# Performance work log

Measured on AMD Instinct MI355X. Metric: run time of the kernel, lower is better.

Reference implementation:

```python
import jax, jax.numpy as jnp
import numpy as np

K = 16
EPS = 1e-5
NEG_SLOPE = 0.2


def leaky(x):
    return jnp.where(x > 0, x, NEG_SLOPE * x)


def batchnorm_train(x, gamma, beta):
    # x: [B, D]; training-mode BN with biased variance (torch semantics)
    mean = jnp.mean(x, axis=0)
    var = jnp.mean((x - mean) ** 2, axis=0)
    return (x - mean) * jax.lax.rsqrt(var + EPS) * gamma + beta


def setup_inputs() -> dict:
    key = jax.random.key(0)
    ks = jax.random.split(key, 20)
    N, M, D = 30000, 8000, 16
    s = lambda fan_in: 1.0 / np.sqrt(fan_in)
    inp = {
        "xyz": jax.random.normal(ks[0], (N, 3), jnp.float32),
        "atom_xyz": jax.random.normal(ks[1], (M, 3), jnp.float32),
        "atom_types": jax.random.normal(ks[2], (M, D), jnp.float32),
        "Wt1": jax.random.uniform(ks[3], (D, D), jnp.float32, -s(D), s(D)),
        "bt1": jax.random.uniform(ks[4], (D,), jnp.float32, -s(D), s(D)),
        "Wt2": jax.random.uniform(ks[5], (D, D), jnp.float32, -s(D), s(D)),
        "bt2": jax.random.uniform(ks[6], (D,), jnp.float32, -s(D), s(D)),
        "Wt3": jax.random.uniform(ks[7], (D, D), jnp.float32, -s(D), s(D)),
        "bt3": jax.random.uniform(ks[8], (D,), jnp.float32, -s(D), s(D)),
        # embed: conv1 Linear(D+1, D), conv2 Linear(D, D), conv3 Linear(2D, D)
        "W1": jax.random.uniform(ks[9], (D + 1, D), jnp.float32, -s(D + 1), s(D + 1)),
        "b1": jax.random.uniform(ks[10], (D,), jnp.float32, -s(D + 1), s(D + 1)),
        "W2": jax.random.uniform(ks[11], (D, D), jnp.float32, -s(D), s(D)),
        "b2": jax.random.uniform(ks[12], (D,), jnp.float32, -s(D), s(D)),
        "W3": jax.random.uniform(ks[13], (2 * D, D), jnp.float32, -s(2 * D), s(2 * D)),
        "b3": jax.random.uniform(ks[14], (D,), jnp.float32, -s(2 * D), s(2 * D)),
        # batchnorm affine params
        "g1": jnp.ones((D,), jnp.float32),
        "be1": jnp.zeros((D,), jnp.float32),
        "g2": jnp.ones((D,), jnp.float32),
        "be2": jnp.zeros((D,), jnp.float32),
    }
    return inp


def reference(xyz, atom_xyz, atom_types,
              Wt1, bt1, Wt2, bt2, Wt3, bt3,
              W1, b1, W2, b2, W3, b3, g1, be1, g2, be2):
    N, D = xyz.shape[0], atom_types.shape[1]

    # transform_types MLP on atom features: [M, D]
    t = leaky(atom_types @ Wt1 + bt1)
    t = leaky(t @ Wt2 + bt2)
    t = leaky(t @ Wt3 + bt3)

    # kNN: squared distances via GEMM expansion (avoids [N,M,3])
    d2 = (jnp.sum(xyz ** 2, axis=1, keepdims=True)
          + jnp.sum(atom_xyz ** 2, axis=1)[None, :]
          - 2.0 * xyz @ atom_xyz.T)                      # [N, M]
    _, idx = jax.lax.top_k(-d2, K)                       # [N, K] nearest atoms

    # gather neighbor coords, recompute exact squared dists (as in source)
    y_ik = atom_xyz[idx]                                 # [N, K, 3]
    dists = jnp.sum((xyz[:, None, :] - y_ik) ** 2, axis=-1)  # [N, K]

    feat = jnp.concatenate([t[idx], (1.0 / dists)[..., None]], axis=-1)  # [N,K,D+1]

    # conv1 -> leaky -> bn1 -> sum-pool
    fx = feat @ W1 + b1                                  # [N, K, D]
    fx = batchnorm_train(leaky(fx).reshape(-1, D), g1, be1).reshape(N, K, D)
    fx1 = fx.sum(axis=1)                                 # [N, D]

    # conv2 -> leaky -> bn2 -> sum-pool
    fx = fx @ W2 + b2
    fx = batchnorm_train(leaky(fx).reshape(-1, D), g2, be2).reshape(N, K, D)
    fx2 = fx.sum(axis=1)                                 # [N, D]

    return jnp.concatenate([fx1, fx2], axis=-1) @ W3 + b3  # [N, D]
```

## Files before the change

### kernel.cpp

```cpp
#include <hip/hip_runtime.h>

#define N_PTS   30000
#define M_ATOMS 8000
#define D       16
#define KNN     16
#define NGRP    125
#define EPS     1e-5f
#define SLOPE   0.2f
#define BN_COUNT 480000.0f

typedef unsigned long long ull;

__device__ __forceinline__ float leaky(float x) { return x > 0.f ? x : SLOPE * x; }

__device__ __forceinline__ unsigned fkey(float f) {
  unsigned u = __float_as_uint(f);
  return u ^ ((u & 0x80000000u) ? 0xFFFFFFFFu : 0x80000000u);
}
__device__ __forceinline__ float unfkey(unsigned e) {
  unsigned u = (e & 0x80000000u) ? (e ^ 0x80000000u) : ~e;
  return __uint_as_float(u);
}

#define DPPSTEP32(v, CTRL) {                                                   \
  unsigned t_ = (unsigned)__builtin_amdgcn_update_dpp(-1, (int)(v), CTRL, 0xF, 0xF, false); \
  (v) = t_ < (v) ? t_ : (v); }

__device__ __forceinline__ unsigned wmin32d(unsigned v) {
  DPPSTEP32(v, 0x111); DPPSTEP32(v, 0x112); DPPSTEP32(v, 0x114);
  DPPSTEP32(v, 0x118); DPPSTEP32(v, 0x142); DPPSTEP32(v, 0x143);
  return (unsigned)__builtin_amdgcn_readlane((int)v, 63);
}

__device__ __forceinline__ void cswap(ull& a, ull& b) {
  ull mn = a < b ? a : b, mx = a < b ? b : a;
  a = mn; b = mx;
}

__device__ __forceinline__ int morton_cell(float x, float y, float z) {
  int cx = min(max((int)floorf((x + 4.f) * 2.f), 0), 15);
  int cy = min(max((int)floorf((y + 4.f) * 2.f), 0), 15);
  int cz = min(max((int)floorf((z + 4.f) * 2.f), 0), 15);
  int c = 0;
#pragma unroll
  for (int b = 0; b < 4; ++b)
    c |= (((cx>>b)&1) << (3*b)) | (((cy>>b)&1) << (3*b+1)) | (((cz>>b)&1) << (3*b+2));
  return c;
}

#define LAYER(IN, OUT, W, B)                                        \
  _Pragma("unroll") for (int j = 0; j < 16; ++j) {                  \
    float acc = B[j];                                               \
    _Pragma("unroll") for (int i = 0; i < 16; ++i)                  \
      acc = fmaf(IN[i], W[i*16+j], acc);                            \
    OUT[j] = leaky(acc);                                            \
  }

__global__ void __launch_bounds__(256) kA_mlp_hist(
    const float* __restrict__ atom_xyz, const float* __restrict__ atom_types,
    const float* __restrict__ Wt1, const float* __restrict__ bt1,
    const float* __restrict__ Wt2, const float* __restrict__ bt2,
    const float* __restrict__ Wt3, const float* __restrict__ bt3,
    const float* __restrict__ W1, const float* __restrict__ b1,
    float* __restrict__ tu_out, int* __restrict__ hist) {
  __shared__ float w1[256], w2[256], w3[256], wc[256];
  __shared__ float bb1[16], bb2[16], bb3[16], bbc[16];
  __shared__ int lh[4096];
  int tid = threadIdx.x;
  for (int i = tid; i < 4096; i += 256) lh[i] = 0;
  w1[tid] = Wt1[tid]; w2[tid] = Wt2[tid]; w3[tid] = Wt3[tid]; wc[tid] = W1[tid];
  if (tid < 16) { bb1[tid] = bt1[tid]; bb2[tid] = bt2[tid];
                  bb3[tid] = bt3[tid]; bbc[tid] = b1[tid]; }
  __syncthreads();
  int m = blockIdx.x * 256 + tid;
  if (m < M_ATOMS) {
    int c = morton_cell(atom_xyz[m*3], atom_xyz[m*3+1], atom_xyz[m*3+2]);
    atomicAdd(&lh[c], 1);

    float u[16], v[16];
    const float4* tp = (const float4*)(atom_types + (size_t)m*16);
    float4 q0 = tp[0], q1 = tp[1], q2 = tp[2], q3 = tp[3];
    u[0]=q0.x; u[1]=q0.y; u[2]=q0.z; u[3]=q0.w;
    u[4]=q1.x; u[5]=q1.y; u[6]=q1.z; u[7]=q1.w;
    u[8]=q2.x; u[9]=q2.y; u[10]=q2.z; u[11]=q2.w;
    u[12]=q3.x; u[13]=q3.y; u[14]=q3.z; u[15]=q3.w;
    LAYER(u, v, w1, bb1);
    LAYER(v, u, w2, bb2);
    LAYER(u, v, w3, bb3);
    float up[16];
#pragma unroll
    for (int j = 0; j < 16; ++j) {
      float acc = bbc[j];
#pragma unroll
      for (int i = 0; i < 16; ++i) acc = fmaf(v[i], wc[i*16+j], acc);
      up[j] = acc;
    }
    float4* op = (float4*)(tu_out + (size_t)m*16);
    op[0] = make_float4(up[0], up[1], up[2], up[3]);
    op[1] = make_float4(up[4], up[5], up[6], up[7]);
    op[2] = make_float4(up[8], up[9], up[10], up[11]);
    op[3] = make_float4(up[12], up[13], up[14], up[15]);
  }
  __syncthreads();
  int* slice = hist + (size_t)blockIdx.x * 4096;
  for (int i = tid; i < 4096; i += 256) slice[i] = lh[i];
}

__global__ void __launch_bounds__(1024) kB_scan(
    const int* __restrict__ hist, int* __restrict__ cursors,
    float* __restrict__ gstats, unsigned* __restrict__ benc) {
  __shared__ int h0[4096], h1[4096];
  int tid = threadIdx.x;
  for (int i = tid; i < 4096; i += 1024) {
    int s = 0;
#pragma unroll
    for (int b = 0; b < 32; ++b) s += hist[b*4096 + i];
    h0[i] = s;
  }
  if (tid < 544) gstats[tid] = 0.f;
  if (tid < 375) benc[tid] = 0xFFFFFFFFu;
  if (tid >= 375 && tid < 750) benc[tid] = 0u;
  __syncthreads();
  int* src = h0; int* dst = h1;
  for (int off = 1; off < 4096; off <<= 1) {
    for (int i = tid; i < 4096; i += 1024) {
      int v = src[i];
      if (i >= off) v += src[i-off];
      dst[i] = v;
    }
    __syncthreads();
    int* t = src; src = dst; dst = t;
  }
  for (int i = tid; i < 4096; i += 1024) cursors[i] = i ? src[i-1] : 0;
}

__global__ void __launch_bounds__(256) kC_scatter(
    const float* __restrict__ atom_xyz, int* __restrict__ cursors,
    float4* __restrict__ atoms4s, int* __restrict__ origid,
    unsigned* __restrict__ benc) {
  int m = blockIdx.x * 256 + threadIdx.x;
  if (m >= M_ATOMS) return;
  float x = atom_xyz[m*3], y = atom_xyz[m*3+1], z = atom_xyz[m*3+2];
  int c = morton_cell(x, y, z);
  int pos = atomicAdd(&cursors[c], 1);
  atoms4s[pos] = make_float4(x, y, z, fmaf(x,x, fmaf(y,y, z*z)));
  origid[pos] = m;
  int g = pos >> 6;
  atomicMin(&benc[g],       fkey(x)); atomicMax(&benc[375+g],     fkey(x));
  atomicMin(&benc[125+g],   fkey(y)); atomicMax(&benc[375+125+g], fkey(y));
  atomicMin(&benc[250+g],   fkey(z)); atomicMax(&benc[375+250+g], fkey(z));
}

__global__ void __launch_bounds__(128) k_dec(
    const unsigned* __restrict__ benc, float4* __restrict__ bounds) {
  int g = threadIdx.x;
  if (g >= NGRP) return;
  bounds[2*g]   = make_float4(unfkey(benc[g]),     unfkey(benc[125+g]),
                              unfkey(benc[250+g]), 0.f);
  bounds[2*g+1] = make_float4(unfkey(benc[375+g]),     unfkey(benc[375+125+g]),
                              unfkey(benc[375+250+g]), 0.f);
}

__global__ void __launch_bounds__(128) k2_knn(
    const float* __restrict__ xyz, const float4* __restrict__ atoms4s,
    const int* __restrict__ origid, const float4* __restrict__ bounds,
    const float* __restrict__ atom_xyz, const float* __restrict__ tu,
    const float* __restrict__ W1,
    int2* __restrict__ pairs, float* __restrict__ gstats) {
  __shared__ float sbuf[2*16*20];
  int tid = threadIdx.x;
  int lane = tid & 63;
  int wid = tid >> 6;
  int n = blockIdx.x * 2 + wid;

  float px = xyz[n*3+0], py = xyz[n*3+1], pz = xyz[n*3+2];
  float x2 = fmaf(px,px, fmaf(py,py, pz*pz));

  unsigned ea, eb = 0xFFFFFFFFu;
  {
    int g = lane;
    float4 mn = bounds[2*g], mx = bounds[2*g+1];
    float dx = fmaxf(fmaxf(mn.x - px, px - mx.x), 0.f);
    float dy = fmaxf(fmaxf(mn.y - py, py - mx.y), 0.f);
    float dz = fmaxf(fmaxf(mn.z - pz, pz - mx.z), 0.f);
    float lb = fmaf(dx,dx, fmaf(dy,dy, dz*dz)) * 0.999f - 1e-4f;
    ea = (fkey(lb) & 0xFFFFFF00u) | (unsigned)g;
  }
  if (lane + 64 < NGRP) {
    int g = lane + 64;
    float4 mn = bounds[2*g], mx = bounds[2*g+1];
    float dx = fmaxf(fmaxf(mn.x - px, px - mx.x), 0.f);
    float dy = fmaxf(fmaxf(mn.y - py, py - mx.y), 0.f);
    float dz = fmaxf(fmaxf(mn.z - pz, pz - mx.z), 0.f);
    float lb = fmaf(dx,dx, fmaf(dy,dy, dz*dz)) * 0.999f - 1e-4f;
    eb = (fkey(lb) & 0xFFFFFF00u) | (unsigned)g;
  }
  unsigned cur = ea < eb ? ea : eb;
  unsigned bak = ea < eb ? eb : ea;

  int gs[4];
#pragma unroll
  for (int r = 0; r < 4; ++r) {
    unsigned m = wmin32d(cur);
    bool own = (cur == m);
    cur = own ? bak : cur;
    bak = own ? 0xFFFFFFFFu : bak;
    gs[r] = (int)(m & 0xFFu);
  }

  float4 A[4]; int OI[4];
#pragma unroll
  for (int r = 0; r < 4; ++r) {
    int base = gs[r] << 6;
    A[r]  = atoms4s[base + lane];
    OI[r] = origid [base + lane];
  }
  ull E[4];
#pragma unroll
  for (int r = 0; r < 4; ++r) {
    float dotp = fmaf(px,A[r].x, fmaf(py,A[r].y, pz*A[r].z));
    float d2 = (x2 + A[r].w) - 2.f*dotp;
    E[r] = ((ull)fkey(d2) << 32) | (unsigned)OI[r];
  }
  cswap(E[0],E[1]); cswap(E[2],E[3]); cswap(E[0],E[2]);
  cswap(E[1],E[3]); cswap(E[1],E[2]);
  unsigned cf0 = (unsigned)(E[0] >> 32), ci0 = (unsigned)E[0];
  unsigned cf1 = (unsigned)(E[1] >> 32), ci1 = (unsigned)E[1];
  unsigned cf2 = (unsigned)(E[2] >> 32), ci2 = (unsigned)E[2];
  unsigned cf3 = (unsigned)(E[3] >> 32), ci3 = (unsigned)E[3];

  ull res = ~0ull;
  unsigned mf = 0, mi = 0;
  for (int r = 0; r < KNN; ++r) {
    mf = wmin32d(cf0);
    ull ball = __ballot(cf0 == mf);
    if (__popcll(ball) == 1) {
      int srcl = (int)(__ffsll(ball) - 1);
      mi = (unsigned)__builtin_amdgcn_readlane((int)ci0, srcl);
    } else {
      unsigned cand = (cf0 == mf) ? ci0 : 0xFFFFFFFFu;
      mi = wmin32d(cand);
    }
    bool own = (cf0 == mf) && (ci0 == mi);
    if (lane == r) res = (((ull)mf) << 32) | mi;
    cf0 = own ? cf1 : cf0; cf1 = own ? cf2 : cf1;
    cf2 = own ? cf3 : cf2; cf3 = own ? 0xFFFFFFFFu : cf3;
    ci0 = own ? ci1 : ci0; ci1 = own ? ci2 : ci1;
    ci2 = own ? ci3 : ci2; ci3 = own ? 0xFFFFFFFFu : ci3;
  }
  ull lv = res;
  ull thresh = (((ull)mf) << 32) | mi;

  for (int it = 0; it < NGRP - 4; ++it) {
    unsigned m = wmin32d(cur);
    if ((m & 0xFFFFFF00u) >= (unsigned)(thresh >> 32)) break;
    bool own = (cur == m);
    cur = own ? bak : cur;
    bak = own ? 0xFFFFFFFFu : bak;
    int base = (int)(m & 0xFFu) << 6;

    float4 a = atoms4s[base + lane];
    int oi2 = origid[base + lane];
    float dotp = fmaf(px,a.x, fmaf(py,a.y, pz*a.z));
    float d2 = (x2 + a.w) - 2.f*dotp;
    ull key = ((ull)fkey(d2) << 32) | (unsigned)oi2;

    ull mk = __ballot(key < thresh);
    while (mk) {
      int src = (int)(__ffsll(mk) - 1);
      mk &= mk - 1;
      unsigned klo = (unsigned)__builtin_amdgcn_readlane((int)(unsigned)key, src);
      unsigned khi = (unsigned)__builtin_amdgcn_readlane((int)(unsigned)(key >> 32), src);
      ull kc = ((ull)khi << 32) | klo;
      if (kc < thresh) {
        bool ins = (lane < KNN) && (kc < lv);
        unsigned pvlo = (unsigned)__builtin_amdgcn_update_dpp(0, (int)(unsigned)lv,        0x111, 0xF, 0xF, false);
        unsigned pvhi = (unsigned)__builtin_amdgcn_update_dpp(0, (int)(unsigned)(lv>>32), 0x111, 0xF, 0xF, false);
        int pins      =           __builtin_amdgcn_update_dpp(0, ins ? 1 : 0,              0x111, 0xF, 0xF, false);
        if (ins) lv = pins ? (((ull)pvhi << 32) | pvlo) : kc;
        unsigned tlo = (unsigned)__builtin_amdgcn_readlane((int)(unsigned)lv, KNN-1);
        unsigned thi = (unsigned)__builtin_amdgcn_readlane((int)(unsigned)(lv >> 32), KNN-1);
        thresh = ((ull)thi << 32) | tlo;
      }
    }
  }

  int oi = (int)(unsigned)(lv & 0xFFFFFFFFull);
  float iv = 0.f;
  if (lane < KNN) {
    float bx = atom_xyz[oi*3+0], by = atom_xyz[oi*3+1], bz = atom_xyz[oi*3+2];
    float dx = px - bx, dy = py - by, dz = pz - bz;
    float dd = fmaf(dx,dx, fmaf(dy,dy, dz*dz));
    iv = 1.f / dd;
    pairs[n*KNN + lane] = make_int2(oi, __float_as_int(iv));

    const float4* up4 = (const float4*)(tu + (size_t)oi*16);
    float4 u0 = up4[0], u1 = up4[1], u2 = up4[2], u3 = up4[3];
    float4* row = (float4*)&sbuf[(wid*16 + lane)*20];
    float4 w;
    w.x = leaky(fmaf(iv, W1[256+ 0], u0.x)); w.y = leaky(fmaf(iv, W1[256+ 1], u0.y));
    w.z = leaky(fmaf(iv, W1[256+ 2], u0.z)); w.w = leaky(fmaf(iv, W1[256+ 3], u0.w));
    row[0] = w;
    w.x = leaky(fmaf(iv, W1[256+ 4], u1.x)); w.y = leaky(fmaf(iv, W1[256+ 5], u1.y));
    w.z = leaky(fmaf(iv, W1[256+ 6], u1.z)); w.w = leaky(fmaf(iv, W1[256+ 7], u1.w));
    row[1] = w;
    w.x = leaky(fmaf(iv, W1[256+ 8], u2.x)); w.y = leaky(fmaf(iv, W1[256+ 9], u2.y));
    w.z = leaky(fmaf(iv, W1[256+10], u2.z)); w.w = leaky(fmaf(iv, W1[256+11], u2.w));
    row[2] = w;
    w.x = leaky(fmaf(iv, W1[256+12], u3.x)); w.y = leaky(fmaf(iv, W1[256+13], u3.y));
    w.z = leaky(fmaf(iv, W1[256+14], u3.z)); w.w = leaky(fmaf(iv, W1[256+15], u3.w));
    row[3] = w;
  }
  __syncthreads();
  {
    int ch = tid & 15, grp = tid >> 4;
    float S = 0.f, Q = 0.f;
#pragma unroll
    for (int i = 0; i < 4; ++i) {
      float v = sbuf[(grp*4 + i)*20 + ch];
      S += v; Q += v*v;
    }
    __syncthreads();
    sbuf[grp*20 + ch] = S;
    sbuf[160 + grp*20 + ch] = Q;
  }
  __syncthreads();
  if (tid < 32) {
    int ch = tid & 15;
    int off = (tid < 16) ? 0 : 160;
    float s = 0.f;
#pragma unroll
    for (int g = 0; g < 8; ++g) s += sbuf[off + g*20 + ch];
    atomicAdd(&gstats[(blockIdx.x & 15)*32 + tid], s);
  }
}

__device__ __forceinline__ void a1_row(const float* __restrict__ tu, int idx,
                                       float iv, const float* wiv, float* a) {
  const float4* up = (const float4*)(tu + (size_t)idx*16);
  float4 r0 = up[0], r1 = up[1], r2 = up[2], r3 = up[3];
  float u[16];
  u[0]=r0.x; u[1]=r0.y; u[2]=r0.z; u[3]=r0.w;
  u[4]=r1.x; u[5]=r1.y; u[6]=r1.z; u[7]=r1.w;
  u[8]=r2.x; u[9]=r2.y; u[10]=r2.z; u[11]=r2.w;
  u[12]=r3.x; u[13]=r3.y; u[14]=r3.z; u[15]=r3.w;
#pragma unroll
  for (int j = 0; j < 16; ++j) a[j] = leaky(fmaf(iv, wiv[j], u[j]));
}

__global__ void __launch_bounds__(256, 4) k4_main(
    const int2* __restrict__ pairs, const float* __restrict__ tu,
    const float* __restrict__ W1,
    const float* __restrict__ W2, const float* __restrict__ b2,
    const float* __restrict__ g1, const float* __restrict__ be1,
    float* __restrict__ fx1_out, float* __restrict__ s2_out,
    float* __restrict__ gstats) {
  __shared__ float wiv[16], w2s[256], b2s[16];
  __shared__ float sc1[16], sh1[16];
  __shared__ float buf[16*16*17];
  int tid = threadIdx.x;
  w2s[tid] = W2[tid];
  if (tid < 16) { wiv[tid] = W1[256 + tid]; b2s[tid] = b2[tid]; }
  if (tid < 16) {
    float s1 = 0.f, q1 = 0.f;
#pragma unroll
    for (int c = 0; c < 16; ++c) { s1 += gstats[c*32 + tid]; q1 += gstats[c*32 + 16 + tid]; }
    float mean = s1 * (1.f/BN_COUNT);
    float var  = q1 * (1.f/BN_COUNT) - mean*mean;
    float sC = g1[tid] / sqrtf(var + EPS);
    sc1[tid] = sC;
    sh1[tid] = be1[tid] - mean * sC;
  }
  __syncthreads();

  int g = blockIdx.x * 256 + tid;
  int p = tid >> 4, k = tid & 15;
  int2 pr = pairs[g];
  int idx = pr.x;
  float iv = __int_as_float(pr.y);
  float h[16], a2[16];
  a1_row(tu, idx, iv, wiv, h);
#pragma unroll
  for (int j = 0; j < 16; ++j) h[j] = fmaf(h[j], sc1[j], sh1[j]);
#pragma unroll
  for (int j = 0; j < 16; ++j) {
    float accj = b2s[j];
#pragma unroll
    for (int i = 0; i < 16; ++i) accj = fmaf(h[i], w2s[i*16+j], accj);
    a2[j] = leaky(accj);
  }

  float* myrow = &buf[(p*16 + k)*17];
  int p2 = tid >> 4, j2 = tid & 15;
#pragma unroll
  for (int j = 0; j < 16; ++j) myrow[j] = h[j];
  __syncthreads();
  {
    float s = 0.f;
#pragma unroll
    for (int kk = 0; kk < 16; ++kk) s += buf[(p2*16+kk)*17 + j2];
    fx1_out[(size_t)blockIdx.x*256 + tid] = s;
  }
  __syncthreads();
#pragma unroll
  for (int j = 0; j < 16; ++j) myrow[j] = a2[j];
  __syncthreads();
  float s2v = 0.f;
#pragma unroll
  for (int kk = 0; kk < 16; ++kk) s2v += buf[(p2*16+kk)*17 + j2];
  s2_out[(size_t)blockIdx.x*256 + tid] = s2v;
  __syncthreads();
#pragma unroll
  for (int j = 0; j < 16; ++j) myrow[j] = a2[j]*a2[j];
  __syncthreads();
  float q2v = 0.f;
#pragma unroll
  for (int kk = 0; kk < 16; ++kk) q2v += buf[(p2*16+kk)*17 + j2];
  __syncthreads();
  buf[p2*17 + j2] = s2v;
  buf[289 + p2*17 + j2] = q2v;
  __syncthreads();
  if (tid < 16) {
    float t1 = 0.f, t2 = 0.f;
#pragma unroll
    for (int pp = 0; pp < 16; ++pp) { t1 += buf[pp*17 + tid]; t2 += buf[289 + pp*17 + tid]; }
    atomicAdd(&gstats[512 + tid], t1);
    atomicAdd(&gstats[528 + tid], t2);
  }
}

__global__ void __launch_bounds__(256) k5_final(
    const float* __restrict__ fx1_in, const float* __restrict__ s2_in,
    const float* __restrict__ gstats,
    const float* __restrict__ W3, const float* __restrict__ b3,
    const float* __restrict__ g2, const float* __restrict__ be2,
    float* __restrict__ out) {
  __shared__ float w[512], bb[16], sc2[16], sh2[16];
  int tid = threadIdx.x;
  w[tid] = W3[tid]; w[256+tid] = W3[256+tid];
  if (tid < 16) {
    bb[tid] = b3[tid];
    float mean = gstats[512+tid] * (1.f/BN_COUNT);
    float var  = gstats[528+tid] * (1.f/BN_COUNT) - mean*mean;
    float s = g2[tid] / sqrtf(var + EPS);
    sc2[tid] = s;
    sh2[tid] = be2[tid] - mean * s;
  }
  __syncthreads();
  int n = blockIdx.x * 256 + tid;
  if (n >= N_PTS) return;

  const float4* f1p = (const float4*)(fx1_in + (size_t)n*16);
  const float4* f2p = (const float4*)(s2_in  + (size_t)n*16);
  float4 x0=f1p[0], x1=f1p[1], x2=f1p[2], x3=f1p[3];
  float4 y0=f2p[0], y1=f2p[1], y2=f2p[2], y3=f2p[3];
  float f1[16] = {x0.x,x0.y,x0.z,x0.w, x1.x,x1.y,x1.z,x1.w,
                  x2.x,x2.y,x2.z,x2.w, x3.x,x3.y,x3.z,x3.w};
  float f2[16] = {y0.x,y0.y,y0.z,y0.w, y1.x,y1.y,y1.z,y1.w,
                  y2.x,y2.y,y2.z,y2.w, y3.x,y3.y,y3.z,y3.w};
#pragma unroll
  for (int i = 0; i < 16; ++i) f2[i] = fmaf(sc2[i], f2[i], 16.f * sh2[i]);

  float4* op = (float4*)(out + (size_t)n*16);
  float o[16];
#pragma unroll
  for (int j = 0; j < 16; ++j) {
    float accj = bb[j];
#pragma unroll
    for (int i = 0; i < 16; ++i) accj = fmaf(f1[i], w[i*16+j], accj);
#pragma unroll
    for (int i = 0; i < 16; ++i) accj = fmaf(f2[i], w[(16+i)*16+j], accj);
    o[j] = accj;
  }
  op[0] = make_float4(o[0], o[1], o[2], o[3]);
  op[1] = make_float4(o[4], o[5], o[6], o[7]);
  op[2] = make_float4(o[8], o[9], o[10], o[11]);
  op[3] = make_float4(o[12], o[13], o[14], o[15]);
}

extern "C" void kernel_launch(void* const* d_in, const int* in_sizes, int n_in,
                              void* d_out, int out_size, void* d_ws, size_t ws_size,
                              hipStream_t stream) {
  const float* xyz        = (const float*)d_in[0];
  const float* atom_xyz   = (const float*)d_in[1];
  const float* atom_types = (const float*)d_in[2];
  const float* Wt1 = (const float*)d_in[3];  const float* bt1 = (const float*)d_in[4];
  const float* Wt2 = (const float*)d_in[5];  const float* bt2 = (const float*)d_in[6];
  const float* Wt3 = (const float*)d_in[7];  const float* bt3 = (const float*)d_in[8];
  const float* W1  = (const float*)d_in[9];  const float* b1  = (const float*)d_in[10];
  const float* W2  = (const float*)d_in[11]; const float* b2  = (const float*)d_in[12];
  const float* W3  = (const float*)d_in[13]; const float* b3  = (const float*)d_in[14];
  const float* g1  = (const float*)d_in[15]; const float* be1 = (const float*)d_in[16];
  const float* g2  = (const float*)d_in[17]; const float* be2 = (const float*)d_in[18];
  float* out = (float*)d_out;

  float* ws = (float*)d_ws;
  float*    tu      = ws;
  int2*     pairs   = (int2*)(ws + 128000);
  float*    fx1     = ws + 1088000;
  float*    s2      = ws + 1568000;
  float*    gstats  = ws + 2048000;
  int*      hist    = (int*)(ws + 2048544);
  int*      cursors = (int*)(ws + 2179616);
  unsigned* benc    = (unsigned*)(ws + 2183712);
  float4*   bounds  = (float4*)(ws + 2184464);
  float4*   atoms4s = (float4*)(ws + 1088000);
  int*      origid  = (int*)(ws + 1120000);

  kA_mlp_hist<<<32, 256, 0, stream>>>(atom_xyz, atom_types, Wt1, bt1, Wt2, bt2,
                                      Wt3, bt3, W1, b1, tu, hist);
  kB_scan<<<1, 1024, 0, stream>>>(hist, cursors, gstats, benc);
  kC_scatter<<<32, 256, 0, stream>>>(atom_xyz, cursors, atoms4s, origid, benc);
  k_dec<<<1, 128, 0, stream>>>(benc, bounds);
  k2_knn<<<15000, 128, 0, stream>>>(xyz, atoms4s, origid, bounds, atom_xyz,
                                    tu, W1, pairs, gstats);
  k4_main<<<1875, 256, 0, stream>>>(pairs, tu, W1, W2, b2, g1, be1,
                                    fx1, s2, gstats);
  k5_final<<<118, 256, 0, stream>>>(fx1, s2, gstats, W3, b3, g2, be2, out);
}
```

Baseline: 229.1 us.

## Merge atom prep kernels into one cooperative kernel with grid syncs

Replaces the four small preprocessing kernels (MLP+histogram, scan, scatter, bounds decode) with one cooperative launch of 32 blocks that separates the phases with grid.sync(). The per-block shared histograms are replaced by one global histogram built with atomics, and block 0 does the scan. The aim is to remove three kernel launch gaps on a tiny prep stage. In exchange it adds grid-wide barriers, more global atomic contention on the bins, and a scan done by 256 threads instead of 1024.

```diff
diff --git a/kernel.cpp b/kernel.cpp
--- a/kernel.cpp
+++ b/kernel.cpp
@@ -1,4 +1,7 @@
 #include <hip/hip_runtime.h>
+#include <hip/hip_cooperative_groups.h>
+
+namespace cg = cooperative_groups;
 
 #define N_PTS   30000
 #define M_ATOMS 8000
@@ -56,26 +59,37 @@
     OUT[j] = leaky(acc);                                            \
   }
 
-__global__ void __launch_bounds__(256) kA_mlp_hist(
+__global__ void kP_prep(
     const float* __restrict__ atom_xyz, const float* __restrict__ atom_types,
     const float* __restrict__ Wt1, const float* __restrict__ bt1,
     const float* __restrict__ Wt2, const float* __restrict__ bt2,
     const float* __restrict__ Wt3, const float* __restrict__ bt3,
     const float* __restrict__ W1, const float* __restrict__ b1,
-    float* __restrict__ tu_out, int* __restrict__ hist) {
+    float* __restrict__ tu_out, int* __restrict__ bins,
+    int* __restrict__ cursors, unsigned* __restrict__ benc,
+    float* __restrict__ gstats, float4* __restrict__ atoms4s,
+    int* __restrict__ origid, float4* __restrict__ bounds) {
+  cg::grid_group grid = cg::this_grid();
   __shared__ float w1[256], w2[256], w3[256], wc[256];
   __shared__ float bb1[16], bb2[16], bb3[16], bbc[16];
-  __shared__ int lh[4096];
+  __shared__ int h0[4096], h1[4096];
   int tid = threadIdx.x;
-  for (int i = tid; i < 4096; i += 256) lh[i] = 0;
+  int gtid = blockIdx.x * 256 + tid;
+
   w1[tid] = Wt1[tid]; w2[tid] = Wt2[tid]; w3[tid] = Wt3[tid]; wc[tid] = W1[tid];
   if (tid < 16) { bb1[tid] = bt1[tid]; bb2[tid] = bt2[tid];
                   bb3[tid] = bt3[tid]; bbc[tid] = b1[tid]; }
-  __syncthreads();
-  int m = blockIdx.x * 256 + tid;
-  if (m < M_ATOMS) {
+
+  if (gtid < 4096) bins[gtid] = 0;
+  if (gtid < 544) gstats[gtid] = 0.f;
+  if (gtid < 375) benc[gtid] = 0xFFFFFFFFu;
+  else if (gtid < 750) benc[gtid] = 0u;
+  grid.sync();
+
+  if (gtid < M_ATOMS) {
+    int m = gtid;
     int c = morton_cell(atom_xyz[m*3], atom_xyz[m*3+1], atom_xyz[m*3+2]);
-    atomicAdd(&lh[c], 1);
+    atomicAdd(&bins[c], 1);
 
     float u[16], v[16];
     const float4* tp = (const float4*)(atom_types + (size_t)m*16);
@@ -101,64 +115,46 @@
     op[2] = make_float4(up[8], up[9], up[10], up[11]);
     op[3] = make_float4(up[12], up[13], up[14], up[15]);
   }
-  __syncthreads();
-  int* slice = hist + (size_t)blockIdx.x * 4096;
-  for (int i = tid; i < 4096; i += 256) slice[i] = lh[i];
-}
-
-__global__ void __launch_bounds__(1024) kB_scan(
-    const int* __restrict__ hist, int* __restrict__ cursors,
-    float* __restrict__ gstats, unsigned* __restrict__ benc) {
-  __shared__ int h0[4096], h1[4096];
-  int tid = threadIdx.x;
-  for (int i = tid; i < 4096; i += 1024) {
-    int s = 0;
-#pragma unroll
-    for (int b = 0; b < 32; ++b) s += hist[b*4096 + i];
-    h0[i] = s;
-  }
-  if (tid < 544) gstats[tid] = 0.f;
-  if (tid < 375) benc[tid] = 0xFFFFFFFFu;
-  if (tid >= 375 && tid < 750) benc[tid] = 0u;
-  __syncthreads();
-  int* src = h0; int* dst = h1;
-  for (int off = 1; off < 4096; off <<= 1) {
-    for (int i = tid; i < 4096; i += 1024) {
-      int v = src[i];
-      if (i >= off) v += src[i-off];
-      dst[i] = v;
+  grid.sync();
+
+  if (blockIdx.x == 0) {
+    for (int i = tid; i < 4096; i += 256) h0[i] = bins[i];
+    __syncthreads();
+    int* src = h0; int* dst = h1;
+    for (int off = 1; off < 4096; off <<= 1) {
+      for (int i = tid; i < 4096; i += 256) {
+        int v = src[i];
+        if (i >= off) v += src[i-off];
+        dst[i] = v;
+      }
+      __syncthreads();
+      int* t = src; src = dst; dst = t;
     }
-    __syncthreads();
-    int* t = src; src = dst; dst = t;
-  }
-  for (int i = tid; i < 4096; i += 1024) cursors[i] = i ? src[i-1] : 0;
-}
-
-__global__ void __launch_bounds__(256) kC_scatter(
-    const float* __restrict__ atom_xyz, int* __restrict__ cursors,
-    float4* __restrict__ atoms4s, int* __restrict__ origid,
-    unsigned* __restrict__ benc) {
-  int m = blockIdx.x * 256 + threadIdx.x;
-  if (m >= M_ATOMS) return;
-  float x = atom_xyz[m*3], y = atom_xyz[m*3+1], z = atom_xyz[m*3+2];
-  int c = morton_cell(x, y, z);
-  int pos = atomicAdd(&cursors[c], 1);
-  atoms4s[pos] = make_float4(x, y, z, fmaf(x,x, fmaf(y,y, z*z)));
-  origid[pos] = m;
-  int g = pos >> 6;
-  atomicMin(&benc[g],       fkey(x)); atomicMax(&benc[375+g],     fkey(x));
-  atomicMin(&benc[125+g],   fkey(y)); atomicMax(&benc[375+125+g], fkey(y));
-  atomicMin(&benc[250+g],   fkey(z)); atomicMax(&benc[375+250+g], fkey(z));
-}
-
-__global__ void __launch_bounds__(128) k_dec(
-    const unsigned* __restrict__ benc, float4* __restrict__ bounds) {
-  int g = threadIdx.x;
-  if (g >= NGRP) return;
-  bounds[2*g]   = make_float4(unfkey(benc[g]),     unfkey(benc[125+g]),
-                              unfkey(benc[250+g]), 0.f);
-  bounds[2*g+1] = make_float4(unfkey(benc[375+g]),     unfkey(benc[375+125+g]),
-                              unfkey(benc[375+250+g]), 0.f);
+    for (int i = tid; i < 4096; i += 256) cursors[i] = i ? src[i-1] : 0;
+  }
+  grid.sync();
+
+  if (gtid < M_ATOMS) {
+    int m = gtid;
+    float x = atom_xyz[m*3], y = atom_xyz[m*3+1], z = atom_xyz[m*3+2];
+    int c = morton_cell(x, y, z);
+    int pos = atomicAdd(&cursors[c], 1);
+    atoms4s[pos] = make_float4(x, y, z, fmaf(x,x, fmaf(y,y, z*z)));
+    origid[pos] = m;
+    int g = pos >> 6;
+    atomicMin(&benc[g],       fkey(x)); atomicMax(&benc[375+g],     fkey(x));
+    atomicMin(&benc[125+g],   fkey(y)); atomicMax(&benc[375+125+g], fkey(y));
+    atomicMin(&benc[250+g],   fkey(z)); atomicMax(&benc[375+250+g], fkey(z));
+  }
+  grid.sync();
+
+  if (gtid < NGRP) {
+    int g = gtid;
+    bounds[2*g]   = make_float4(unfkey(benc[g]),     unfkey(benc[125+g]),
+                                unfkey(benc[250+g]), 0.f);
+    bounds[2*g+1] = make_float4(unfkey(benc[375+g]),     unfkey(benc[375+125+g]),
+                                unfkey(benc[375+250+g]), 0.f);
+  }
 }
 
 __global__ void __launch_bounds__(128) k2_knn(
@@ -500,18 +496,23 @@
   float*    fx1     = ws + 1088000;
   float*    s2      = ws + 1568000;
   float*    gstats  = ws + 2048000;
-  int*      hist    = (int*)(ws + 2048544);
-  int*      cursors = (int*)(ws + 2179616);
-  unsigned* benc    = (unsigned*)(ws + 2183712);
-  float4*   bounds  = (float4*)(ws + 2184464);
+  int*      bins    = (int*)(ws + 2048544);
+  int*      cursors = (int*)(ws + 2052640);
+  unsigned* benc    = (unsigned*)(ws + 2056736);
+  float4*   bounds  = (float4*)(ws + 2057488);
   float4*   atoms4s = (float4*)(ws + 1088000);
   int*      origid  = (int*)(ws + 1120000);
 
-  kA_mlp_hist<<<32, 256, 0, stream>>>(atom_xyz, atom_types, Wt1, bt1, Wt2, bt2,
-                                      Wt3, bt3, W1, b1, tu, hist);
-  kB_scan<<<1, 1024, 0, stream>>>(hist, cursors, gstats, benc);
-  kC_scatter<<<32, 256, 0, stream>>>(atom_xyz, cursors, atoms4s, origid, benc);
-  k_dec<<<1, 128, 0, stream>>>(benc, bounds);
+  void* kpArgs[] = {
+    (void*)&atom_xyz, (void*)&atom_types,
+    (void*)&Wt1, (void*)&bt1, (void*)&Wt2, (void*)&bt2,
+    (void*)&Wt3, (void*)&bt3, (void*)&W1, (void*)&b1,
+    (void*)&tu, (void*)&bins, (void*)&cursors, (void*)&benc,
+    (void*)&gstats, (void*)&atoms4s, (void*)&origid, (void*)&bounds
+  };
+  hipLaunchCooperativeKernel((const void*)kP_prep, dim3(32), dim3(256),
+                             kpArgs, 0, stream);
+
   k2_knn<<<15000, 128, 0, stream>>>(xyz, atoms4s, origid, bounds, atom_xyz,
                                     tu, W1, pairs, gstats);
   k4_main<<<1875, 256, 0, stream>>>(pairs, tu, W1, W2, b2, g1, be1,
```

Result: slower. 277.4 us (+21.1%).
